# Kernel tuning notes

Measured on AMD Instinct MI355X. Metric: run time of the kernel, lower is better.

Reference implementation:

```python
import jax, jax.numpy as jnp
import numpy as np

N_NODES = 50000
N_EDGES = 800000
IN_DIM = 128
HIDDEN = 128
OUT_DIM = 40


def setup_inputs() -> dict:
    key = jax.random.key(0)
    ks = jax.random.split(key, 6)
    x = jax.random.normal(ks[0], (N_NODES, IN_DIM), dtype=jnp.float32)
    edge_src = jax.random.randint(ks[1], (N_EDGES,), 0, N_NODES, dtype=jnp.int32)
    edge_dst = jax.random.randint(ks[2], (N_EDGES,), 0, N_NODES, dtype=jnp.int32)
    edge_weight = jax.random.uniform(ks[3], (N_EDGES,), dtype=jnp.float32)
    W1 = jax.random.normal(ks[4], (IN_DIM, HIDDEN), dtype=jnp.float32) / np.sqrt(IN_DIM)
    b1 = jnp.zeros((HIDDEN,), dtype=jnp.float32)
    W2 = jax.random.normal(ks[5], (HIDDEN, OUT_DIM), dtype=jnp.float32) / np.sqrt(HIDDEN)
    b2 = jnp.zeros((OUT_DIM,), dtype=jnp.float32)
    return {"x": x, "edge_src": edge_src, "edge_dst": edge_dst,
            "edge_weight": edge_weight, "W1": W1, "b1": b1, "W2": W2, "b2": b2}


def _spmm(edge_src, edge_dst, edge_weight, x):
    # out[i] = sum_{e: dst==i} w_e * x[src_e]   (sparse adj @ x)
    msgs = edge_weight[:, None] * x[edge_src]  # [E, D] gather
    return jax.ops.segment_sum(msgs, edge_dst, num_segments=N_NODES)


def reference(x, edge_src, edge_dst, edge_weight, W1, b1, W2, b2):
    # dropout p=0.0 (eval): identity
    h = _spmm(edge_src, edge_dst, edge_weight, x)       # adj @ x
    h = jax.nn.relu(h @ W1 + b1)                        # lin1 + relu
    h = _spmm(edge_src, edge_dst, edge_weight, h)       # adj @ h
    return h @ W2 + b2                                  # lin2
```

## Files before the change

### kernel.cpp

```cpp
#include <hip/hip_runtime.h>
#include <hip/hip_bf16.h>

#define N_NODES 50000
#define N_EDGES 800000
#define IN_DIM 128
#define HIDDEN 128
#define OUT_DIM 40
#define G_STRIDE 64

#define SCAN_BS 1024
#define SCAN_BLOCKS ((N_NODES + SCAN_BS - 1) / SCAN_BS)

#define N_COPIES 8
#define HIST_STRIDE 50176
#define FLAG_BASE 50000

#define HIST_BLOCKS 3128
#define G1_BLOCKS ((N_NODES + 63) / 64)
#define HG_GRID 3910

struct __align__(8) Edge { int s; float w; };

typedef __attribute__((ext_vector_type(8))) short bf16x8;
typedef __attribute__((ext_vector_type(4))) float f32x4;
typedef __attribute__((ext_vector_type(8))) unsigned short u16x8;
typedef __attribute__((ext_vector_type(4))) unsigned short u16x4;

__device__ __forceinline__ unsigned f32_to_bf16_bits(float f) {
    unsigned u = __float_as_uint(f);
    return (u + 0x7FFFu + ((u >> 16) & 1u)) >> 16;
}
__device__ __forceinline__ float b2f(unsigned short u) {
    return __uint_as_float(((unsigned)u) << 16);
}
__device__ __forceinline__ int src_slice(int s) {
    return (int)((unsigned)s / 6250u);
}

__global__ __launch_bounds__(256) void hist_gemm1(const int* __restrict__ dst,
                                                  const int* __restrict__ srcv,
                                                  int* __restrict__ hist8,
                                                  unsigned short* __restrict__ erank,
                                                  const float* __restrict__ x,
                                                  const float* __restrict__ W1,
                                                  __hip_bfloat16* __restrict__ y)
{
    __shared__ bf16x8 w1s[2048];
    int bid = blockIdx.x;

    if ((bid % 5) != 4) {
        int hb = bid - bid / 5;
        int i = hb * 256 + threadIdx.x;
        if (i < N_EDGES) {
            int copy = src_slice(srcv[i]);
            erank[i] = (unsigned short)atomicAdd(&hist8[copy * HIST_STRIDE + dst[i]], 1);
        }
        return;
    }

    int gb = bid / 5;
    int t = threadIdx.x;
    for (int f = t; f < 2048; f += 256) {
        int lane = f & 63;
        int nt = (f >> 6) & 7;
        int ks = f >> 9;
        int m = lane & 15, quad = lane >> 4;
        bf16x8 frag;
        #pragma unroll
        for (int j = 0; j < 8; ++j) {
            int k = ks * 32 + quad * 8 + j;
            frag[j] = (short)f32_to_bf16_bits(W1[k * HIDDEN + nt * 16 + m]);
        }
        w1s[f] = frag;
    }
    __syncthreads();

    int wv = t >> 6;
    int lane = t & 63;
    int m = lane & 15, quad = lane >> 4;
    int row0 = gb * 64 + wv * 16;
    int arow = row0 + m;
    if (arow >= N_NODES) arow = N_NODES - 1;

    bf16x8 afrag[4];
    #pragma unroll
    for (int ks = 0; ks < 4; ++ks) {
        const float4* xp = (const float4*)(x + (long long)arow * IN_DIM + ks * 32 + quad * 8);
        float4 a0 = xp[0], a1 = xp[1];
        afrag[ks][0] = (short)f32_to_bf16_bits(a0.x);
        afrag[ks][1] = (short)f32_to_bf16_bits(a0.y);
        afrag[ks][2] = (short)f32_to_bf16_bits(a0.z);
        afrag[ks][3] = (short)f32_to_bf16_bits(a0.w);
        afrag[ks][4] = (short)f32_to_bf16_bits(a1.x);
        afrag[ks][5] = (short)f32_to_bf16_bits(a1.y);
        afrag[ks][6] = (short)f32_to_bf16_bits(a1.z);
        afrag[ks][7] = (short)f32_to_bf16_bits(a1.w);
    }

    f32x4 acc[8];
    #pragma unroll
    for (int nt = 0; nt < 8; ++nt) acc[nt] = (f32x4){0.f, 0.f, 0.f, 0.f};

    #pragma unroll
    for (int ks = 0; ks < 4; ++ks) {
        #pragma unroll
        for (int nt = 0; nt < 8; ++nt) {
            bf16x8 bfrag = w1s[(ks * 8 + nt) * 64 + lane];
            acc[nt] = __builtin_amdgcn_mfma_f32_16x16x32_bf16(afrag[ks], bfrag, acc[nt], 0, 0, 0);
        }
    }

    #pragma unroll
    for (int nt = 0; nt < 8; ++nt) {
        #pragma unroll
        for (int r = 0; r < 4; ++r) {
            int rrow = row0 + quad * 4 + r;
            if (rrow < N_NODES)
                y[(long long)rrow * HIDDEN + nt * 16 + m] = __float2bfloat16(acc[nt][r]);
        }
    }
}

__global__ __launch_bounds__(SCAN_BS) void scan_fused(int* __restrict__ hist8,
                                                      int* __restrict__ row_ptr)
{
    __shared__ int tmp[SCAN_BS];
    __shared__ int red[SCAN_BS / 64];
    __shared__ int blk_off;
    int t = threadIdx.x;
    int bid = blockIdx.x;
    int i = bid * SCAN_BS + t;

    int total = 0;
    if (i < N_NODES) {
        int off = 0;
        #pragma unroll
        for (int c = 0; c < N_COPIES; ++c) {
            int h = hist8[c * HIST_STRIDE + i];
            hist8[c * HIST_STRIDE + i] = off;
            off += h;
        }
        total = off;
    }
    int s = total;
    for (int off = 32; off > 0; off >>= 1) s += __shfl_down(s, off, 64);
    int wave = t >> 6, lane = t & 63;
    if (lane == 0) red[wave] = s;
    __syncthreads();
    if (t == 0) {
        int tt = 0;
        #pragma unroll
        for (int wv = 0; wv < SCAN_BS / 64; ++wv) tt += red[wv];
        __hip_atomic_store(&hist8[FLAG_BASE + bid], tt + 1,
                           __ATOMIC_RELEASE, __HIP_MEMORY_SCOPE_AGENT);
    }
    if (t < 64) {
        int v2 = 0;
        if (t < bid) {
            int v;
            do {
                v = __hip_atomic_load(&hist8[FLAG_BASE + t],
                                      __ATOMIC_ACQUIRE, __HIP_MEMORY_SCOPE_AGENT);
            } while (v == 0);
            v2 = v - 1;
        }
        for (int off = 32; off > 0; off >>= 1) v2 += __shfl_down(v2, off, 64);
        if (t == 0) {
            blk_off = v2;
            if (bid == 0) row_ptr[N_NODES] = N_EDGES;
        }
    }
    int v = total;
    tmp[t] = v;
    __syncthreads();
    for (int off = 1; off < SCAN_BS; off <<= 1) {
        int u = (t >= off) ? tmp[t - off] : 0;
        __syncthreads();
        tmp[t] += u;
        __syncthreads();
    }
    if (i < N_NODES) row_ptr[i] = tmp[t] - v + blk_off;
}

__global__ __launch_bounds__(256) void scatter_det(const int* __restrict__ src,
                                                   const int* __restrict__ dst,
                                                   const float* __restrict__ w,
                                                   const int* __restrict__ hist8,
                                                   const unsigned short* __restrict__ erank,
                                                   const int* __restrict__ row_ptr,
                                                   Edge* __restrict__ edges)
{
    int i = blockIdx.x * 256 + threadIdx.x;
    int d = dst[i];
    int s = src[i];
    int copy = src_slice(s);
    int pos = row_ptr[d] + hist8[copy * HIST_STRIDE + d] + (int)erank[i];
    Edge ed; ed.s = s; ed.w = w[i];
    edges[pos] = ed;
}

__global__ __launch_bounds__(256) void spmm1_kernel(const int* __restrict__ row_ptr,
                                                    const Edge* __restrict__ edges,
                                                    const __hip_bfloat16* __restrict__ y,
                                                    const float* __restrict__ b1,
                                                    __hip_bfloat16* __restrict__ h1)
{
    int wv = threadIdx.x >> 6;
    int lane = threadIdx.x & 63;
    int grp = lane >> 4;
    int sub = lane & 15;
    int node = blockIdx.x * 16 + wv * 4 + grp;
    int j = row_ptr[node];
    int e = row_ptr[node + 1];

    float acc[8];
    #pragma unroll
    for (int k = 0; k < 8; ++k) acc[k] = 0.f;

    for (; j + 7 < e; j += 8) {
        Edge ed[8];
        #pragma unroll
        for (int u = 0; u < 8; ++u) ed[u] = edges[j + u];
        u16x8 v[8];
        #pragma unroll
        for (int u = 0; u < 8; ++u)
            v[u] = *(const u16x8*)(y + ((long long)ed[u].s << 7) + (sub << 3));
        #pragma unroll
        for (int u = 0; u < 8; ++u) {
            #pragma unroll
            for (int k = 0; k < 8; ++k)
                acc[k] = fmaf(ed[u].w, b2f(v[u][k]), acc[k]);
        }
    }
    for (; j + 3 < e; j += 4) {
        Edge ed[4];
        #pragma unroll
        for (int u = 0; u < 4; ++u) ed[u] = edges[j + u];
        u16x8 v[4];
        #pragma unroll
        for (int u = 0; u < 4; ++u)
            v[u] = *(const u16x8*)(y + ((long long)ed[u].s << 7) + (sub << 3));
        #pragma unroll
        for (int u = 0; u < 4; ++u) {
            #pragma unroll
            for (int k = 0; k < 8; ++k)
                acc[k] = fmaf(ed[u].w, b2f(v[u][k]), acc[k]);
        }
    }
    for (; j < e; ++j) {
        Edge ed0 = edges[j];
        u16x8 v0 = *(const u16x8*)(y + ((long long)ed0.s << 7) + (sub << 3));
        #pragma unroll
        for (int k = 0; k < 8; ++k)
            acc[k] = fmaf(ed0.w, b2f(v0[k]), acc[k]);
    }

    float4 bA = *(const float4*)(b1 + (sub << 3));
    float4 bB = *(const float4*)(b1 + (sub << 3) + 4);
    u16x8 hv;
    hv[0] = (unsigned short)f32_to_bf16_bits(fmaxf(acc[0] + bA.x, 0.f));
    hv[1] = (unsigned short)f32_to_bf16_bits(fmaxf(acc[1] + bA.y, 0.f));
    hv[2] = (unsigned short)f32_to_bf16_bits(fmaxf(acc[2] + bA.z, 0.f));
    hv[3] = (unsigned short)f32_to_bf16_bits(fmaxf(acc[3] + bA.w, 0.f));
    hv[4] = (unsigned short)f32_to_bf16_bits(fmaxf(acc[4] + bB.x, 0.f));
    hv[5] = (unsigned short)f32_to_bf16_bits(fmaxf(acc[5] + bB.y, 0.f));
    hv[6] = (unsigned short)f32_to_bf16_bits(fmaxf(acc[6] + bB.z, 0.f));
    hv[7] = (unsigned short)f32_to_bf16_bits(fmaxf(acc[7] + bB.w, 0.f));
    *(u16x8*)(h1 + ((long long)node << 7) + (sub << 3)) = hv;
}

__global__ __launch_bounds__(256) void gemm2_mfma(const __hip_bfloat16* __restrict__ h1,
                                                  const float* __restrict__ W2,
                                                  __hip_bfloat16* __restrict__ g)
{
    __shared__ bf16x8 w2s[768];
    int t = threadIdx.x;
    for (int f = t; f < 768; f += 256) {
        int lane = f & 63;
        int nt = (f >> 6) % 3;
        int ks = f / 192;
        int m = lane & 15, quad = lane >> 4;
        int col = nt * 16 + m;
        bf16x8 frag;
        #pragma unroll
        for (int j = 0; j < 8; ++j) {
            int k = ks * 32 + quad * 8 + j;
            float val = (col < OUT_DIM) ? W2[k * OUT_DIM + col] : 0.f;
            frag[j] = (short)f32_to_bf16_bits(val);
        }
        w2s[f] = frag;
    }
    __syncthreads();

    int wv = t >> 6;
    int lane = t & 63;
    int m = lane & 15, quad = lane >> 4;
    int row0 = blockIdx.x * 64 + wv * 16;
    int arow = row0 + m;
    if (arow >= N_NODES) arow = N_NODES - 1;

    bf16x8 afrag[4];
    #pragma unroll
    for (int ks = 0; ks < 4; ++ks)
        afrag[ks] = *(const bf16x8*)(h1 + (long long)arow * HIDDEN + ks * 32 + quad * 8);

    f32x4 acc[3];
    #pragma unroll
    for (int nt = 0; nt < 3; ++nt) acc[nt] = (f32x4){0.f, 0.f, 0.f, 0.f};

    #pragma unroll
    for (int ks = 0; ks < 4; ++ks) {
        #pragma unroll
        for (int nt = 0; nt < 3; ++nt) {
            bf16x8 bfrag = w2s[(ks * 3 + nt) * 64 + lane];
            acc[nt] = __builtin_amdgcn_mfma_f32_16x16x32_bf16(afrag[ks], bfrag, acc[nt], 0, 0, 0);
        }
    }

    #pragma unroll
    for (int nt = 0; nt < 3; ++nt) {
        int col = nt * 16 + m;
        if (col < OUT_DIM) {
            #pragma unroll
            for (int r = 0; r < 4; ++r) {
                int rrow = row0 + quad * 4 + r;
                if (rrow < N_NODES)
                    g[(rrow << 6) + col] = __float2bfloat16(acc[nt][r]);
            }
        }
    }
    if (m < 6) {
        u16x4 z = (u16x4){0, 0, 0, 0};
        #pragma unroll
        for (int r = 0; r < 4; ++r) {
            int rrow = row0 + quad * 4 + r;
            if (rrow < N_NODES)
                *(u16x4*)(g + (rrow << 6) + OUT_DIM + m * 4) = z;
        }
    }
}

__global__ __launch_bounds__(256) void spmm2_kernel(const int* __restrict__ row_ptr,
                                                    const Edge* __restrict__ edges,
                                                    const __hip_bfloat16* __restrict__ g,
                                                    const float* __restrict__ b2,
                                                    float* __restrict__ out)
{
    int wv = threadIdx.x >> 6;
    int lane = threadIdx.x & 63;
    int grp = lane >> 4;
    int sub = lane & 15;
    int node = blockIdx.x * 16 + wv * 4 + grp;
    int j = row_ptr[node];
    int e = row_ptr[node + 1];

    float acc[4];
    #pragma unroll
    for (int k = 0; k < 4; ++k) acc[k] = 0.f;

    for (; j + 7 < e; j += 8) {
        Edge ed[8];
        #pragma unroll
        for (int u = 0; u < 8; ++u) ed[u] = edges[j + u];
        u16x4 v[8];
        #pragma unroll
        for (int u = 0; u < 8; ++u)
            v[u] = *(const u16x4*)(g + ((long long)ed[u].s << 6) + (sub << 2));
        #pragma unroll
        for (int u = 0; u < 8; ++u) {
            #pragma unroll
            for (int k = 0; k < 4; ++k)
                acc[k] = fmaf(ed[u].w, b2f(v[u][k]), acc[k]);
        }
    }
    for (; j + 3 < e; j += 4) {
        Edge ed[4];
        #pragma unroll
        for (int u = 0; u < 4; ++u) ed[u] = edges[j + u];
        u16x4 v[4];
        #pragma unroll
        for (int u = 0; u < 4; ++u)
            v[u] = *(const u16x4*)(g + ((long long)ed[u].s << 6) + (sub << 2));
        #pragma unroll
        for (int u = 0; u < 4; ++u) {
            #pragma unroll
            for (int k = 0; k < 4; ++k)
                acc[k] = fmaf(ed[u].w, b2f(v[u][k]), acc[k]);
        }
    }
    for (; j < e; ++j) {
        Edge ed0 = edges[j];
        u16x4 v0 = *(const u16x4*)(g + ((long long)ed0.s << 6) + (sub << 2));
        #pragma unroll
        for (int k = 0; k < 4; ++k)
            acc[k] = fmaf(ed0.w, b2f(v0[k]), acc[k]);
    }

    if (sub < 10) {
        float4 bb = *(const float4*)(b2 + (sub << 2));
        float4 o;
        o.x = acc[0] + bb.x;
        o.y = acc[1] + bb.y;
        o.z = acc[2] + bb.z;
        o.w = acc[3] + bb.w;
        *(float4*)(out + (long long)node * OUT_DIM + (sub << 2)) = o;
    }
}

extern "C" void kernel_launch(void* const* d_in, const int* in_sizes, int n_in,
                              void* d_out, int out_size, void* d_ws, size_t ws_size,
                              hipStream_t stream)
{
    const float* x    = (const float*)d_in[0];
    const int*   esrc = (const int*)  d_in[1];
    const int*   edst = (const int*)  d_in[2];
    const float* ew   = (const float*)d_in[3];
    const float* W1   = (const float*)d_in[4];
    const float* b1   = (const float*)d_in[5];
    const float* W2   = (const float*)d_in[6];
    const float* b2   = (const float*)d_in[7];
    float* out = (float*)d_out;

    __hip_bfloat16* y  = (__hip_bfloat16*)d_ws;
    __hip_bfloat16* g  = y;
    __hip_bfloat16* h1 = y + (size_t)N_NODES * HIDDEN;
    Edge* edges     = (Edge*)(h1 + (size_t)N_NODES * HIDDEN);
    int* hist8      = (int*)(edges + N_EDGES);
    unsigned short* erank = (unsigned short*)(hist8 + N_COPIES * HIST_STRIDE);
    int* row_ptr    = (int*)(erank + N_EDGES);

    hipMemsetAsync(hist8, 0, N_COPIES * HIST_STRIDE * sizeof(int), stream);
    hist_gemm1<<<HG_GRID, 256, 0, stream>>>(edst, esrc, hist8, erank, x, W1, y);
    scan_fused<<<SCAN_BLOCKS, SCAN_BS, 0, stream>>>(hist8, row_ptr);
    scatter_det<<<N_EDGES / 256, 256, 0, stream>>>(esrc, edst, ew, hist8,
                                                   erank, row_ptr, edges);

    spmm1_kernel<<<N_NODES / 16, 256, 0, stream>>>(row_ptr, edges, y, b1, h1);
    gemm2_mfma<<<G1_BLOCKS, 256, 0, stream>>>(h1, W2, g);
    spmm2_kernel<<<N_NODES / 16, 256, 0, stream>>>(row_ptr, edges, g, b2, out);
}
```

Measured before the change: 202.1 us.

## Replace global atomic histogram with per-chunk LDS byte-packed counts

```diff
diff --git a/kernel.cpp b/kernel.cpp
--- a/kernel.cpp
+++ b/kernel.cpp
@@ -11,13 +11,15 @@
 #define SCAN_BS 1024
 #define SCAN_BLOCKS ((N_NODES + SCAN_BS - 1) / SCAN_BS)
 
-#define N_COPIES 8
-#define HIST_STRIDE 50176
-#define FLAG_BASE 50000
-
-#define HIST_BLOCKS 3128
-#define G1_BLOCKS ((N_NODES + 63) / 64)
-#define HG_GRID 3910
+#define CHUNK_SHIFT 13
+#define CHUNK 8192
+#define NCHUNK 98
+#define CNT_STRIDE 50176
+#define CNT_WORDS (CNT_STRIDE / 4)
+
+#define G1_ROWS 128
+#define G1_BLOCKS ((N_NODES + G1_ROWS - 1) / G1_ROWS)
+#define HG_GRID (NCHUNK + G1_BLOCKS)
 
 struct __align__(8) Edge { int s; float w; };
 
@@ -33,34 +35,41 @@
 __device__ __forceinline__ float b2f(unsigned short u) {
     return __uint_as_float(((unsigned)u) << 16);
 }
-__device__ __forceinline__ int src_slice(int s) {
-    return (int)((unsigned)s / 6250u);
-}
-
-__global__ __launch_bounds__(256) void hist_gemm1(const int* __restrict__ dst,
-                                                  const int* __restrict__ srcv,
-                                                  int* __restrict__ hist8,
-                                                  unsigned short* __restrict__ erank,
+
+__global__ __launch_bounds__(512) void hist_gemm1(const int* __restrict__ dst,
+                                                  unsigned char* __restrict__ cnt,
+                                                  unsigned char* __restrict__ erank,
                                                   const float* __restrict__ x,
                                                   const float* __restrict__ W1,
                                                   __hip_bfloat16* __restrict__ y)
 {
-    __shared__ bf16x8 w1s[2048];
+    __shared__ __align__(16) unsigned int shmem[CNT_WORDS];
     int bid = blockIdx.x;
-
-    if ((bid % 5) != 4) {
-        int hb = bid - bid / 5;
-        int i = hb * 256 + threadIdx.x;
-        if (i < N_EDGES) {
-            int copy = src_slice(srcv[i]);
-            erank[i] = (unsigned short)atomicAdd(&hist8[copy * HIST_STRIDE + dst[i]], 1);
-        }
+    int t = threadIdx.x;
+
+    if (bid < NCHUNK) {
+        for (int f = t; f < CNT_WORDS; f += 512) shmem[f] = 0u;
+        __syncthreads();
+        int base = bid << CHUNK_SHIFT;
+        #pragma unroll
+        for (int r = 0; r < CHUNK / 512; ++r) {
+            int i = base + r * 512 + t;
+            if (i < N_EDGES) {
+                int d = dst[i];
+                unsigned sh = (unsigned)(d & 3) * 8u;
+                unsigned old = atomicAdd(&shmem[d >> 2], 1u << sh);
+                erank[i] = (unsigned char)((old >> sh) & 0xffu);
+            }
+        }
+        __syncthreads();
+        unsigned int* cw = (unsigned int*)(cnt + (size_t)bid * CNT_STRIDE);
+        for (int f = t; f < CNT_WORDS; f += 512) cw[f] = shmem[f];
         return;
     }
 
-    int gb = bid / 5;
-    int t = threadIdx.x;
-    for (int f = t; f < 2048; f += 256) {
+    bf16x8* w1s = (bf16x8*)shmem;
+    int gb = bid - NCHUNK;
+    for (int f = t; f < 2048; f += 512) {
         int lane = f & 63;
         int nt = (f >> 6) & 7;
         int ks = f >> 9;
@@ -78,7 +87,7 @@
     int wv = t >> 6;
     int lane = t & 63;
     int m = lane & 15, quad = lane >> 4;
-    int row0 = gb * 64 + wv * 16;
+    int row0 = gb * G1_ROWS + wv * 16;
     int arow = row0 + m;
     if (arow >= N_NODES) arow = N_NODES - 1;
 
@@ -121,8 +130,9 @@
     }
 }
 
-__global__ __launch_bounds__(SCAN_BS) void scan_fused(int* __restrict__ hist8,
-                                                      int* __restrict__ row_ptr)
+__global__ __launch_bounds__(SCAN_BS) void scan_fused(unsigned char* __restrict__ cnt,
+                                                      int* __restrict__ row_ptr,
+                                                      int* __restrict__ flags)
 {
     __shared__ int tmp[SCAN_BS];
     __shared__ int red[SCAN_BS / 64];
@@ -134,10 +144,9 @@
     int total = 0;
     if (i < N_NODES) {
         int off = 0;
-        #pragma unroll
-        for (int c = 0; c < N_COPIES; ++c) {
-            int h = hist8[c * HIST_STRIDE + i];
-            hist8[c * HIST_STRIDE + i] = off;
+        for (int c = 0; c < NCHUNK; ++c) {
+            unsigned char h = cnt[(size_t)c * CNT_STRIDE + i];
+            cnt[(size_t)c * CNT_STRIDE + i] = (unsigned char)off;
             off += h;
         }
         total = off;
@@ -151,7 +160,7 @@
         int tt = 0;
         #pragma unroll
         for (int wv = 0; wv < SCAN_BS / 64; ++wv) tt += red[wv];
-        __hip_atomic_store(&hist8[FLAG_BASE + bid], tt + 1,
+        __hip_atomic_store(&flags[bid], tt + 1,
                            __ATOMIC_RELEASE, __HIP_MEMORY_SCOPE_AGENT);
     }
     if (t < 64) {
@@ -159,7 +168,7 @@
         if (t < bid) {
             int v;
             do {
-                v = __hip_atomic_load(&hist8[FLAG_BASE + t],
+                v = __hip_atomic_load(&flags[t],
                                       __ATOMIC_ACQUIRE, __HIP_MEMORY_SCOPE_AGENT);
             } while (v == 0);
             v2 = v - 1;
@@ -185,17 +194,16 @@
 __global__ __launch_bounds__(256) void scatter_det(const int* __restrict__ src,
                                                    const int* __restrict__ dst,
                                                    const float* __restrict__ w,
-                                                   const int* __restrict__ hist8,
-                                                   const unsigned short* __restrict__ erank,
+                                                   const unsigned char* __restrict__ cnt,
+                                                   const unsigned char* __restrict__ erank,
                                                    const int* __restrict__ row_ptr,
                                                    Edge* __restrict__ edges)
 {
     int i = blockIdx.x * 256 + threadIdx.x;
     int d = dst[i];
-    int s = src[i];
-    int copy = src_slice(s);
-    int pos = row_ptr[d] + hist8[copy * HIST_STRIDE + d] + (int)erank[i];
-    Edge ed; ed.s = s; ed.w = w[i];
+    int chunk = i >> CHUNK_SHIFT;
+    int pos = row_ptr[d] + (int)cnt[(size_t)chunk * CNT_STRIDE + d] + (int)erank[i];
+    Edge ed; ed.s = src[i]; ed.w = w[i];
     edges[pos] = ed;
 }
 
@@ -425,17 +433,18 @@
     __hip_bfloat16* g  = y;
     __hip_bfloat16* h1 = y + (size_t)N_NODES * HIDDEN;
     Edge* edges     = (Edge*)(h1 + (size_t)N_NODES * HIDDEN);
-    int* hist8      = (int*)(edges + N_EDGES);
-    unsigned short* erank = (unsigned short*)(hist8 + N_COPIES * HIST_STRIDE);
+    unsigned char* cnt   = (unsigned char*)(edges + N_EDGES);
+    unsigned char* erank = cnt + (size_t)NCHUNK * CNT_STRIDE;
     int* row_ptr    = (int*)(erank + N_EDGES);
-
-    hipMemsetAsync(hist8, 0, N_COPIES * HIST_STRIDE * sizeof(int), stream);
-    hist_gemm1<<<HG_GRID, 256, 0, stream>>>(edst, esrc, hist8, erank, x, W1, y);
-    scan_fused<<<SCAN_BLOCKS, SCAN_BS, 0, stream>>>(hist8, row_ptr);
-    scatter_det<<<N_EDGES / 256, 256, 0, stream>>>(esrc, edst, ew, hist8,
+    int* flags      = row_ptr + 50176;
+
+    hipMemsetAsync(flags, 0, 64 * sizeof(int), stream);
+    hist_gemm1<<<HG_GRID, 512, 0, stream>>>(edst, cnt, erank, x, W1, y);
+    scan_fused<<<SCAN_BLOCKS, SCAN_BS, 0, stream>>>(cnt, row_ptr, flags);
+    scatter_det<<<N_EDGES / 256, 256, 0, stream>>>(esrc, edst, ew, cnt,
                                                    erank, row_ptr, edges);
 
     spmm1_kernel<<<N_NODES / 16, 256, 0, stream>>>(row_ptr, edges, y, b1, h1);
-    gemm2_mfma<<<G1_BLOCKS, 256, 0, stream>>>(h1, W2, g);
+    gemm2_mfma<<<(N_NODES + 63) / 64, 256, 0, stream>>>(h1, W2, g);
     spmm2_kernel<<<N_NODES / 16, 256, 0, stream>>>(row_ptr, edges, g, b2, out);
 }
```

Result: faster. 181.3 us, median of 2 (-10.3%).
